# Kernel tuning notes

Measured on AMD Instinct MI355X. Metric: run time of the kernel, lower is better.

The kernel has to match this reference:

```python
import jax, jax.numpy as jnp
import numpy as np

NUM_CLASSES = 1000
FEATURE_DIM = 1024
BATCH = 8192
MOMENTUM = 0.9
LAMBDA_INTRA = 1.0
LAMBDA_INTER = 0.5


def setup_inputs() -> dict:
    key = jax.random.key(0)
    k1, k2, k3, k4 = jax.random.split(key, 4)
    return {
        "features": jax.random.normal(k1, (BATCH, FEATURE_DIM), jnp.float32),
        "features_adv": jax.random.normal(k2, (BATCH, FEATURE_DIM), jnp.float32),
        "centers": jax.random.normal(k3, (NUM_CLASSES, FEATURE_DIM), jnp.float32),
        "labels": jax.random.randint(k4, (BATCH,), 0, NUM_CLASSES, dtype=jnp.int64),
    }


def _l2_normalize(x):
    # torch F.normalize(p=2, dim=1) with eps=1e-12 clamp on the norm
    n = jnp.linalg.norm(x, axis=1, keepdims=True)
    return x / jnp.maximum(n, 1e-12)


def _update_centers(centers, feats, labels):
    # Vectorized version of the per-class masked-mean momentum update.
    C = centers.shape[0]
    sums = jax.ops.segment_sum(feats, labels, num_segments=C)            # [C, D]
    counts = jax.ops.segment_sum(jnp.ones((feats.shape[0],), feats.dtype), labels, num_segments=C)  # [C]
    means = sums / jnp.maximum(counts, 1.0)[:, None]
    has_samples = (counts > 0)[:, None]
    center_is_zero = jnp.all(centers == 0, axis=1, keepdims=True)
    updated = jnp.where(center_is_zero, means, MOMENTUM * centers + (1.0 - MOMENTUM) * means)
    return jnp.where(has_samples, updated, centers)


def reference(features, features_adv, centers, labels):
    f = _l2_normalize(features)
    fa = _l2_normalize(features_adv)

    # update_centers runs under no_grad on detached normalized features
    centers_new = _update_centers(centers, jax.lax.stop_gradient(f), labels)

    centers_batch = centers_new[labels]  # [B, D] gather
    intra_clean = jnp.linalg.norm(f - centers_batch, axis=1).mean()
    intra_adv = jnp.linalg.norm(fa - centers_batch, axis=1).mean()

    # fused pairwise center distances: ||ci||^2 + ||cj||^2 - 2 ci.cj
    sq = jnp.sum(centers_new * centers_new, axis=1)                      # [C]
    d2 = sq[:, None] + sq[None, :] - 2.0 * (centers_new @ centers_new.T)  # [C, C]
    dist = jnp.sqrt(jnp.maximum(d2, 0.0))
    C = centers_new.shape[0]
    upper = jnp.triu(jnp.ones((C, C), dtype=bool), k=1)
    n_pairs = C * (C - 1) / 2.0
    inter_loss = jnp.sum(jnp.where(upper, jax.nn.relu(1.0 - dist), 0.0)) / n_pairs

    return LAMBDA_INTRA * (intra_clean + intra_adv) - LAMBDA_INTER * inter_loss
```

## Files before the change

### kernel.cpp

```cpp
#include <hip/hip_runtime.h>
#include <math.h>

#define BATCH 8192
#define DIM 1024
#define NCLS 1000
#define NPAD 1024
#define NPAIRS 499500.0f

typedef float  f32x4  __attribute__((ext_vector_type(4)));
typedef short  bf16x8 __attribute__((ext_vector_type(8)));


__device__ inline float waveAllReduceAdd(float x) {
  #pragma unroll
  for (int m = 32; m > 0; m >>= 1) x += __shfl_xor(x, m);
  return x;
}

__device__ inline float blockReduce1(float x, float* sm) {
  x = waveAllReduceAdd(x);
  int lane = threadIdx.x & 63, wid = threadIdx.x >> 6;
  __syncthreads();
  if (lane == 0) sm[wid] = x;
  __syncthreads();
  return sm[0] + sm[1] + sm[2] + sm[3];
}

__device__ inline unsigned short f2bf(float f) {
  unsigned int u = __float_as_uint(f);
  u += 0x7FFFu + ((u >> 16) & 1u);
  return (unsigned short)(u >> 16);
}


__global__ void norms_kernel(const float* __restrict__ feats, float* __restrict__ invn) {
  int lane = threadIdx.x & 63;
  int row = blockIdx.x * 4 + (threadIdx.x >> 6);
  const float4* f4 = (const float4*)(feats + (size_t)row * DIM);
  float ss = 0.f;
  #pragma unroll
  for (int i = 0; i < 4; ++i) {
    float4 v = f4[lane + 64 * i];
    ss += v.x * v.x + v.y * v.y + v.z * v.z + v.w * v.w;
  }
  ss = waveAllReduceAdd(ss);
  if (lane == 0) invn[row] = 1.0f / fmaxf(sqrtf(ss), 1e-12f);
}


__global__ void hist_scan_scatter_kernel(const int* __restrict__ labels, int* counts,
                                         int* offsets, int* rows_sorted,
                                         float* partials) {
  __shared__ int h[1024];
  __shared__ int cur[1024];
  int t = threadIdx.x;
  h[t] = 0;
  if (t < 768) partials[t] = 0.0f;
  __syncthreads();
  #pragma unroll
  for (int j = t; j < BATCH; j += 1024) atomicAdd(&h[labels[j]], 1);
  __syncthreads();
  int v = h[t];
  if (t < NCLS) counts[t] = v;
  for (int off = 1; off < 1024; off <<= 1) {
    int u = (t >= off) ? h[t - off] : 0;
    __syncthreads();
    h[t] += u;
    __syncthreads();
  }
  int e = h[t] - v;
  cur[t] = e;
  if (t < NCLS) offsets[t] = e;
  __syncthreads();
  #pragma unroll
  for (int j = t; j < BATCH; j += 1024) {
    int pos = atomicAdd(&cur[labels[j]], 1);
    rows_sorted[pos] = j;
  }
}


__global__ void update_centers_kernel(const float* __restrict__ feats,
                                      const float* __restrict__ centers,
                                      const int* __restrict__ counts,
                                      const int* __restrict__ offsets,
                                      const int* __restrict__ rows_sorted,
                                      const float* __restrict__ invn,
                                      unsigned short* __restrict__ centers_bf,
                                      float* __restrict__ sqn) {
  __shared__ float sm[8];
  __shared__ int s_anynz;
  int c = blockIdx.x;
  int tid = threadIdx.x;
  int fi = tid;

  if (c >= NCLS) {
    ((ushort4*)(centers_bf + (size_t)c * DIM))[fi] = make_ushort4(0, 0, 0, 0);
    return;
  }

  int n = counts[c];
  int off = offsets[c];

  float4 acc = make_float4(0.f, 0.f, 0.f, 0.f);
  for (int t = 0; t < n; ++t) {
    int r = rows_sorted[off + t];
    float w = invn[r];
    float4 v = ((const float4*)(feats + (size_t)r * DIM))[fi];
    acc.x += v.x * w; acc.y += v.y * w; acc.z += v.z * w; acc.w += v.w * w;
  }
  float invc = 1.0f / fmaxf((float)n, 1.0f);
  float4 mean = make_float4(acc.x * invc, acc.y * invc, acc.z * invc, acc.w * invc);

  float4 cv = ((const float4*)(centers + (size_t)c * DIM))[fi];
  if (tid == 0) s_anynz = 0;
  __syncthreads();
  if (cv.x != 0.f || cv.y != 0.f || cv.z != 0.f || cv.w != 0.f) s_anynz = 1;
  __syncthreads();

  float4 o;
  if (s_anynz) {
    o = make_float4(0.9f * cv.x + 0.1f * mean.x, 0.9f * cv.y + 0.1f * mean.y,
                    0.9f * cv.z + 0.1f * mean.z, 0.9f * cv.w + 0.1f * mean.w);
  } else {
    o = mean;
  }
  if (n == 0) o = cv;

  ((ushort4*)(centers_bf + (size_t)c * DIM))[fi] =
      make_ushort4(f2bf(o.x), f2bf(o.y), f2bf(o.z), f2bf(o.w));

  float sq = blockReduce1(o.x * o.x + o.y * o.y + o.z * o.z + o.w * o.w, sm);
  if (tid == 0) sqn[c] = sq;
}


__global__ void intra_kernel(const float* __restrict__ feats,
                             const float* __restrict__ featsa,
                             const unsigned short* __restrict__ centers_bf,
                             const int* __restrict__ labels,
                             const float* __restrict__ invn,
                             float* __restrict__ partials) {
  int lane = threadIdx.x & 63;
  int row = blockIdx.x * 4 + (threadIdx.x >> 6);
  const float4* f4 = (const float4*)(feats + (size_t)row * DIM);
  const float4* a4 = (const float4*)(featsa + (size_t)row * DIM);
  int lab = labels[row];
  const ushort4* c4 = (const ushort4*)(centers_bf + (size_t)lab * DIM);

  float4 fv[4], av[4];
  ushort4 cv[4];
  float ssa = 0.f;
  #pragma unroll
  for (int i = 0; i < 4; ++i) {
    fv[i] = f4[lane + 64 * i];
    av[i] = a4[lane + 64 * i];
    cv[i] = c4[lane + 64 * i];
    ssa += av[i].x * av[i].x + av[i].y * av[i].y + av[i].z * av[i].z + av[i].w * av[i].w;
  }
  ssa = waveAllReduceAdd(ssa);
  float inva = 1.0f / fmaxf(sqrtf(ssa), 1e-12f);
  float invf = invn[row];

  float d2c = 0.f, d2a = 0.f;
  #pragma unroll
  for (int i = 0; i < 4; ++i) {
    float cx = __uint_as_float((unsigned)cv[i].x << 16);
    float cy = __uint_as_float((unsigned)cv[i].y << 16);
    float cz = __uint_as_float((unsigned)cv[i].z << 16);
    float cw = __uint_as_float((unsigned)cv[i].w << 16);
    float dx = fv[i].x * invf - cx, dy = fv[i].y * invf - cy;
    float dz = fv[i].z * invf - cz, dw = fv[i].w * invf - cw;
    d2c += dx * dx + dy * dy + dz * dz + dw * dw;
    float ex = av[i].x * inva - cx, ey = av[i].y * inva - cy;
    float ez = av[i].z * inva - cz, ew = av[i].w * inva - cw;
    d2a += ex * ex + ey * ey + ez * ez + ew * ew;
  }
  d2c = waveAllReduceAdd(d2c);
  d2a = waveAllReduceAdd(d2a);
  if (lane == 0) {
    int slot = row & 255;
    atomicAdd(&partials[slot], sqrtf(d2c));
    atomicAdd(&partials[256 + slot], sqrtf(d2a));
  }
}


__global__ void inter_mfma_kernel(const unsigned short* __restrict__ Cbf,
                                  const float* __restrict__ sq,
                                  float* __restrict__ inter_partial) {
  int bi = blockIdx.y, bj = blockIdx.x;
  if (bj < bi) return;

  __shared__ float smr[8];
  int tid = threadIdx.x;
  int w = tid >> 6;
  int wy = w >> 1, wx = w & 1;
  int lane = tid & 63;
  int m = lane & 15;
  int q = lane >> 4;

  int i0 = bi * 64 + wy * 32;
  int j0 = bj * 64 + wx * 32;

  const unsigned short* arow0 = Cbf + (size_t)(i0 + m) * DIM;
  const unsigned short* arow1 = Cbf + (size_t)(i0 + 16 + m) * DIM;
  const unsigned short* brow0 = Cbf + (size_t)(j0 + m) * DIM;
  const unsigned short* brow1 = Cbf + (size_t)(j0 + 16 + m) * DIM;

  f32x4 acc00 = {0.f, 0.f, 0.f, 0.f}, acc01 = acc00, acc10 = acc00, acc11 = acc00;

  #pragma unroll 4
  for (int k0 = 0; k0 < DIM; k0 += 32) {
    int ko = k0 + q * 8;
    bf16x8 a0 = *(const bf16x8*)(arow0 + ko);
    bf16x8 a1 = *(const bf16x8*)(arow1 + ko);
    bf16x8 b0 = *(const bf16x8*)(brow0 + ko);
    bf16x8 b1 = *(const bf16x8*)(brow1 + ko);
    acc00 = __builtin_amdgcn_mfma_f32_16x16x32_bf16(a0, b0, acc00, 0, 0, 0);
    acc01 = __builtin_amdgcn_mfma_f32_16x16x32_bf16(a0, b1, acc01, 0, 0, 0);
    acc10 = __builtin_amdgcn_mfma_f32_16x16x32_bf16(a1, b0, acc10, 0, 0, 0);
    acc11 = __builtin_amdgcn_mfma_f32_16x16x32_bf16(a1, b1, acc11, 0, 0, 0);
  }

  float local = 0.f;
  int colA = lane & 15;
  int rbase = (lane >> 4) * 4;
  #pragma unroll
  for (int si = 0; si < 2; ++si) {
    #pragma unroll
    for (int sj = 0; sj < 2; ++sj) {
      f32x4 a = (si == 0) ? (sj == 0 ? acc00 : acc01) : (sj == 0 ? acc10 : acc11);
      #pragma unroll
      for (int r = 0; r < 4; ++r) {
        int i = i0 + si * 16 + rbase + r;
        int j = j0 + sj * 16 + colA;
        if (j < NCLS && i < j) {
          float d2 = sq[i] + sq[j] - 2.0f * a[r];
          float d = sqrtf(fmaxf(d2, 0.0f));
          local += fmaxf(1.0f - d, 0.0f);
        }
      }
    }
  }
  float tot = blockReduce1(local, smr);
  if (tid == 0) atomicAdd(&inter_partial[(bi * 16 + bj) & 255], tot);
}


__global__ void final_kernel(const float* __restrict__ partials, float* __restrict__ out) {
  __shared__ float sm[8];
  int t = threadIdx.x;
  float c = partials[t] + partials[256 + t];
  float e = partials[512 + t];
  c = blockReduce1(c, sm);
  e = blockReduce1(e, sm);
  if (t == 0) {
    float intra = c * (1.0f / (float)BATCH);
    float inter = e / NPAIRS;
    out[0] = intra - 0.5f * inter;
  }
}


extern "C" void kernel_launch(void* const* d_in, const int* in_sizes, int n_in,
                              void* d_out, int out_size, void* d_ws, size_t ws_size,
                              hipStream_t stream) {
  const float* features     = (const float*)d_in[0];
  const float* features_adv = (const float*)d_in[1];
  const float* centers      = (const float*)d_in[2];
  const int*   labels       = (const int*)d_in[3];
  float* out = (float*)d_out;

  unsigned short* centers_bf = (unsigned short*)d_ws;
  float* sqn = (float*)(centers_bf + (size_t)NPAD * DIM);
  float* invn = sqn + NCLS;
  float* partials = invn + BATCH;
  int* counts = (int*)(partials + 768);
  int* offsets = counts + NCLS;
  int* rows_sorted = offsets + NCLS;

  hipLaunchKernelGGL(norms_kernel, dim3(BATCH / 4), dim3(256), 0, stream,
                     features, invn);
  hipLaunchKernelGGL(hist_scan_scatter_kernel, dim3(1), dim3(1024), 0, stream, labels,
                     counts, offsets, rows_sorted, partials);
  hipLaunchKernelGGL(update_centers_kernel, dim3(NPAD), dim3(256), 0, stream, features,
                     centers, counts, offsets, rows_sorted, invn, centers_bf, sqn);
  hipLaunchKernelGGL(intra_kernel, dim3(BATCH / 4), dim3(256), 0, stream, features,
                     features_adv, centers_bf, labels, invn, partials);
  hipLaunchKernelGGL(inter_mfma_kernel, dim3(16, 16), dim3(256), 0, stream, centers_bf,
                     sqn, partials + 512);
  hipLaunchKernelGGL(final_kernel, dim3(1), dim3(256), 0, stream, partials, out);
}
```

Before: 155.6 us.

## Replace sort-based center update with atomic scatter-add and fuse intra/inter kernels

Drops the single-block histogram/scan/scatter kernel and the per-class gather loop. Each row now scatters its normalized features into a per-class sum buffer with float atomics, alongside the norm computation. The intra and inter (MFMA) passes are merged into one launch, and the inter tiles are remapped to only the upper-triangle blocks so no blocks exit early. This removes a serial single-block kernel and two launches, at the cost of 8M float atomics into an extra 4MB workspace plus a zeroing kernel. Float atomics also make the summation order nondeterministic.

```diff
diff --git a/kernel.cpp b/kernel.cpp
--- a/kernel.cpp
+++ b/kernel.cpp
@@ -6,6 +6,8 @@
 #define NCLS 1000
 #define NPAD 1024
 #define NPAIRS 499500.0f
+#define NTILE 136
+#define GINTRA 2048
 
 typedef float  f32x4  __attribute__((ext_vector_type(4)));
 typedef short  bf16x8 __attribute__((ext_vector_type(8)));
@@ -33,66 +35,60 @@
 }
 
 
-__global__ void norms_kernel(const float* __restrict__ feats, float* __restrict__ invn) {
+__global__ void zero_kernel(float* __restrict__ sums, int* __restrict__ counts,
+                            float* __restrict__ partials) {
+  int i = blockIdx.x * 256 + threadIdx.x;
+  float4* s4 = (float4*)sums;
+  const int n4 = NCLS * DIM / 4;
+  if (i < n4) s4[i] = make_float4(0.f, 0.f, 0.f, 0.f);
+  if (i < NCLS) counts[i] = 0;
+  if (i < 768) partials[i] = 0.0f;
+}
+
+
+__global__ void norm_accum_kernel(const float* __restrict__ feats,
+                                  const int* __restrict__ labels,
+                                  float* __restrict__ invn,
+                                  float* __restrict__ sums,
+                                  int* __restrict__ counts) {
   int lane = threadIdx.x & 63;
   int row = blockIdx.x * 4 + (threadIdx.x >> 6);
   const float4* f4 = (const float4*)(feats + (size_t)row * DIM);
+  float4 v[4];
   float ss = 0.f;
   #pragma unroll
   for (int i = 0; i < 4; ++i) {
-    float4 v = f4[lane + 64 * i];
-    ss += v.x * v.x + v.y * v.y + v.z * v.z + v.w * v.w;
+    v[i] = f4[lane + 64 * i];
+    ss += v[i].x * v[i].x + v[i].y * v[i].y + v[i].z * v[i].z + v[i].w * v[i].w;
   }
   ss = waveAllReduceAdd(ss);
-  if (lane == 0) invn[row] = 1.0f / fmaxf(sqrtf(ss), 1e-12f);
-}
-
-
-__global__ void hist_scan_scatter_kernel(const int* __restrict__ labels, int* counts,
-                                         int* offsets, int* rows_sorted,
-                                         float* partials) {
-  __shared__ int h[1024];
-  __shared__ int cur[1024];
-  int t = threadIdx.x;
-  h[t] = 0;
-  if (t < 768) partials[t] = 0.0f;
-  __syncthreads();
-  #pragma unroll
-  for (int j = t; j < BATCH; j += 1024) atomicAdd(&h[labels[j]], 1);
-  __syncthreads();
-  int v = h[t];
-  if (t < NCLS) counts[t] = v;
-  for (int off = 1; off < 1024; off <<= 1) {
-    int u = (t >= off) ? h[t - off] : 0;
-    __syncthreads();
-    h[t] += u;
-    __syncthreads();
-  }
-  int e = h[t] - v;
-  cur[t] = e;
-  if (t < NCLS) offsets[t] = e;
-  __syncthreads();
-  #pragma unroll
-  for (int j = t; j < BATCH; j += 1024) {
-    int pos = atomicAdd(&cur[labels[j]], 1);
-    rows_sorted[pos] = j;
-  }
-}
-
-
-__global__ void update_centers_kernel(const float* __restrict__ feats,
-                                      const float* __restrict__ centers,
-                                      const int* __restrict__ counts,
-                                      const int* __restrict__ offsets,
-                                      const int* __restrict__ rows_sorted,
-                                      const float* __restrict__ invn,
-                                      unsigned short* __restrict__ centers_bf,
-                                      float* __restrict__ sqn) {
+  float inv = 1.0f / fmaxf(sqrtf(ss), 1e-12f);
+  int lab = labels[row];
+  float* dst = sums + (size_t)lab * DIM;
+  #pragma unroll
+  for (int i = 0; i < 4; ++i) {
+    int base = 4 * (lane + 64 * i);
+    atomicAdd(dst + base + 0, v[i].x * inv);
+    atomicAdd(dst + base + 1, v[i].y * inv);
+    atomicAdd(dst + base + 2, v[i].z * inv);
+    atomicAdd(dst + base + 3, v[i].w * inv);
+  }
+  if (lane == 0) {
+    invn[row] = inv;
+    atomicAdd(&counts[lab], 1);
+  }
+}
+
+
+__global__ void center_kernel(const float* __restrict__ sums,
+                              const int* __restrict__ counts,
+                              const float* __restrict__ centers,
+                              unsigned short* __restrict__ centers_bf,
+                              float* __restrict__ sqn) {
   __shared__ float sm[8];
   __shared__ int s_anynz;
   int c = blockIdx.x;
-  int tid = threadIdx.x;
-  int fi = tid;
+  int fi = threadIdx.x;
 
   if (c >= NCLS) {
     ((ushort4*)(centers_bf + (size_t)c * DIM))[fi] = make_ushort4(0, 0, 0, 0);
@@ -100,20 +96,12 @@
   }
 
   int n = counts[c];
-  int off = offsets[c];
-
-  float4 acc = make_float4(0.f, 0.f, 0.f, 0.f);
-  for (int t = 0; t < n; ++t) {
-    int r = rows_sorted[off + t];
-    float w = invn[r];
-    float4 v = ((const float4*)(feats + (size_t)r * DIM))[fi];
-    acc.x += v.x * w; acc.y += v.y * w; acc.z += v.z * w; acc.w += v.w * w;
-  }
+  float4 s = ((const float4*)(sums + (size_t)c * DIM))[fi];
   float invc = 1.0f / fmaxf((float)n, 1.0f);
-  float4 mean = make_float4(acc.x * invc, acc.y * invc, acc.z * invc, acc.w * invc);
+  float4 mean = make_float4(s.x * invc, s.y * invc, s.z * invc, s.w * invc);
 
   float4 cv = ((const float4*)(centers + (size_t)c * DIM))[fi];
-  if (tid == 0) s_anynz = 0;
+  if (fi == 0) s_anynz = 0;
   __syncthreads();
   if (cv.x != 0.f || cv.y != 0.f || cv.z != 0.f || cv.w != 0.f) s_anynz = 1;
   __syncthreads();
@@ -131,18 +119,18 @@
       make_ushort4(f2bf(o.x), f2bf(o.y), f2bf(o.z), f2bf(o.w));
 
   float sq = blockReduce1(o.x * o.x + o.y * o.y + o.z * o.z + o.w * o.w, sm);
-  if (tid == 0) sqn[c] = sq;
-}
-
-
-__global__ void intra_kernel(const float* __restrict__ feats,
-                             const float* __restrict__ featsa,
-                             const unsigned short* __restrict__ centers_bf,
-                             const int* __restrict__ labels,
-                             const float* __restrict__ invn,
-                             float* __restrict__ partials) {
+  if (fi == 0) sqn[c] = sq;
+}
+
+
+__device__ void intra_body(const float* __restrict__ feats,
+                           const float* __restrict__ featsa,
+                           const unsigned short* __restrict__ centers_bf,
+                           const int* __restrict__ labels,
+                           const float* __restrict__ invn,
+                           float* __restrict__ partials, int b) {
   int lane = threadIdx.x & 63;
-  int row = blockIdx.x * 4 + (threadIdx.x >> 6);
+  int row = b * 4 + (threadIdx.x >> 6);
   const float4* f4 = (const float4*)(feats + (size_t)row * DIM);
   const float4* a4 = (const float4*)(featsa + (size_t)row * DIM);
   int lab = labels[row];
@@ -185,12 +173,12 @@
   }
 }
 
-
-__global__ void inter_mfma_kernel(const unsigned short* __restrict__ Cbf,
-                                  const float* __restrict__ sq,
-                                  float* __restrict__ inter_partial) {
-  int bi = blockIdx.y, bj = blockIdx.x;
-  if (bj < bi) return;
+__device__ void inter_body(const unsigned short* __restrict__ Cbf,
+                           const float* __restrict__ sq,
+                           float* __restrict__ inter_partial, int t) {
+  int bi = 0, rem = t;
+  while (rem >= 16 - bi) { rem -= 16 - bi; ++bi; }
+  int bj = bi + rem;
 
   __shared__ float smr[8];
   int tid = threadIdx.x;
@@ -244,7 +232,22 @@
     }
   }
   float tot = blockReduce1(local, smr);
-  if (tid == 0) atomicAdd(&inter_partial[(bi * 16 + bj) & 255], tot);
+  if (tid == 0) atomicAdd(&inter_partial[t & 255], tot);
+}
+
+__global__ void intra_inter_kernel(const float* __restrict__ feats,
+                                   const float* __restrict__ featsa,
+                                   const unsigned short* __restrict__ centers_bf,
+                                   const int* __restrict__ labels,
+                                   const float* __restrict__ invn,
+                                   const float* __restrict__ sqn,
+                                   float* __restrict__ partials) {
+  int b = blockIdx.x;
+  if (b < GINTRA) {
+    intra_body(feats, featsa, centers_bf, labels, invn, partials, b);
+  } else {
+    inter_body(centers_bf, sqn, partials + 512, b - GINTRA);
+  }
 }
 
 
@@ -273,22 +276,19 @@
   float* out = (float*)d_out;
 
   unsigned short* centers_bf = (unsigned short*)d_ws;
-  float* sqn = (float*)(centers_bf + (size_t)NPAD * DIM);
+  float* sums = (float*)(centers_bf + (size_t)NPAD * DIM);
+  float* sqn = sums + (size_t)NCLS * DIM;
   float* invn = sqn + NCLS;
   float* partials = invn + BATCH;
   int* counts = (int*)(partials + 768);
-  int* offsets = counts + NCLS;
-  int* rows_sorted = offsets + NCLS;
-
-  hipLaunchKernelGGL(norms_kernel, dim3(BATCH / 4), dim3(256), 0, stream,
-                     features, invn);
-  hipLaunchKernelGGL(hist_scan_scatter_kernel, dim3(1), dim3(1024), 0, stream, labels,
-                     counts, offsets, rows_sorted, partials);
-  hipLaunchKernelGGL(update_centers_kernel, dim3(NPAD), dim3(256), 0, stream, features,
-                     centers, counts, offsets, rows_sorted, invn, centers_bf, sqn);
-  hipLaunchKernelGGL(intra_kernel, dim3(BATCH / 4), dim3(256), 0, stream, features,
-                     features_adv, centers_bf, labels, invn, partials);
-  hipLaunchKernelGGL(inter_mfma_kernel, dim3(16, 16), dim3(256), 0, stream, centers_bf,
-                     sqn, partials + 512);
+
+  hipLaunchKernelGGL(zero_kernel, dim3(1024), dim3(256), 0, stream, sums, counts,
+                     partials);
+  hipLaunchKernelGGL(norm_accum_kernel, dim3(BATCH / 4), dim3(256), 0, stream,
+                     features, labels, invn, sums, counts);
+  hipLaunchKernelGGL(center_kernel, dim3(NPAD), dim3(256), 0, stream, sums, counts,
+                     centers, centers_bf, sqn);
+  hipLaunchKernelGGL(intra_inter_kernel, dim3(GINTRA + NTILE), dim3(256), 0, stream,
+                     features, features_adv, centers_bf, labels, invn, sqn, partials);
   hipLaunchKernelGGL(final_kernel, dim3(1), dim3(256), 0, stream, partials, out);
 }
```

Result: slower. 250.1 us (+60.8%).
